# Kernel tuning notes

Measured on AMD Instinct MI355X. Metric: run time of the kernel, lower is better.

The kernel has to match this reference:

```python
import jax, jax.numpy as jnp
import numpy as np

B, N, DIM, CD, K = 8, 4096, 1024, 512, 8192


def setup_inputs() -> dict:
    key = jax.random.key(0)
    k0, k1, k2, k3, k4, k5 = jax.random.split(key, 6)
    s_in = 1.0 / np.sqrt(DIM)
    s_out = 1.0 / np.sqrt(CD)
    return {
        "x": jax.random.normal(k0, (B, N, DIM), dtype=jnp.float32),
        "W_in": jax.random.uniform(k1, (DIM, CD), jnp.float32, -s_in, s_in),
        "b_in": jax.random.uniform(k2, (CD,), jnp.float32, -s_in, s_in),
        "embed": jax.random.normal(k3, (K, CD), dtype=jnp.float32),
        "W_out": jax.random.uniform(k4, (CD, DIM), jnp.float32, -s_out, s_out),
        "b_out": jax.random.uniform(k5, (DIM,), jnp.float32, -s_out, s_out),
    }


def reference(x, W_in, b_in, embed, W_out, b_out):
    # project_in: [B,N,DIM] -> [B,N,CD]
    xp = jnp.einsum('bnd,dc->bnc', x, W_in) + b_in
    flat = xp.reshape(-1, CD)  # [B*N, CD]
    # Euclidean codebook: dist = -||flat - embed||^2 (argmax == nearest code)
    dist = (2.0 * flat @ embed.T
            - jnp.sum(flat * flat, axis=-1, keepdims=True)
            - jnp.sum(embed * embed, axis=-1))  # [B*N, K]
    ind = jnp.argmax(dist, axis=-1)  # [B*N]
    quant = embed[ind].reshape(B, N, CD)
    # commitment loss (training path): mse(quantize.detach(), x_projected)
    commit_loss = jnp.mean(jnp.square(jax.lax.stop_gradient(quant) - xp))
    # straight-through estimator
    quant_st = xp + jax.lax.stop_gradient(quant - xp)
    # project_out: [B,N,CD] -> [B,N,DIM]
    out = jnp.einsum('bnc,cd->bnd', quant_st, W_out) + b_out
    return out, ind.reshape(B, N), commit_loss
```

## Files before the change

### kernel.cpp

```cpp
#include <hip/hip_runtime.h>
#include <hip/hip_bf16.h>
#include <math.h>

#define DIMq 1024
#define CDq  512
#define Kq   8192
#define Mq   32768

#define TAU      1.0e-2f
#define FLAGCAP  4096

typedef __attribute__((ext_vector_type(8))) short bf16x8;
typedef __attribute__((ext_vector_type(4))) float f32x4;
typedef __attribute__((ext_vector_type(4))) unsigned short u16x4;

__device__ __forceinline__ ushort bf16rne(float v) {
  unsigned u = __float_as_uint(v);
  return (ushort)((u + 0x7FFFu + ((u >> 16) & 1u)) >> 16);
}
__device__ __forceinline__ float bf16tof(ushort h) {
  return __uint_as_float(((unsigned)h) << 16);
}

__global__ __launch_bounds__(256) void embed_conv_kernel(const float* __restrict__ e,
                                                         ushort* __restrict__ eh,
                                                         ushort* __restrict__ el) {
  size_t i = ((size_t)blockIdx.x * 256 + threadIdx.x) * 8;
  float4 v0 = *(const float4*)(e + i);
  float4 v1 = *(const float4*)(e + i + 4);
  float vv[8] = {v0.x, v0.y, v0.z, v0.w, v1.x, v1.y, v1.z, v1.w};
  u16x4 h0, h1, l0, l1;
#pragma unroll
  for (int j = 0; j < 4; ++j) {
    ushort hb = bf16rne(vv[j]);     h0[j] = hb; l0[j] = bf16rne(vv[j] - bf16tof(hb));
    ushort hc = bf16rne(vv[4 + j]); h1[j] = hc; l1[j] = bf16rne(vv[4 + j] - bf16tof(hc));
  }
  *(u16x4*)(eh + i) = h0; *(u16x4*)(eh + i + 4) = h1;
  *(u16x4*)(el + i) = l0; *(u16x4*)(el + i + 4) = l1;
}

__global__ __launch_bounds__(256) void seminorm_kernel(const float* __restrict__ embed,
                                                       float* __restrict__ sem) {
  int wid  = blockIdx.x * 4 + (threadIdx.x >> 6);
  int lane = threadIdx.x & 63;
  const float* e = embed + (size_t)wid * CDq;
  double s = 0.0;
#pragma unroll
  for (int j = 0; j < 2; ++j) {
    float4 v = *(const float4*)(e + j * 256 + lane * 4);
    s += (double)v.x * v.x + (double)v.y * v.y + (double)v.z * v.z + (double)v.w * v.w;
  }
#pragma unroll
  for (int off = 32; off; off >>= 1) s += __shfl_down(s, off, 64);
  if (lane == 0) sem[wid] = (float)(0.5 * s);
}

__global__ __launch_bounds__(256) void proj_in_kernel(
    const float* __restrict__ A, const float* __restrict__ Bw,
    const float* __restrict__ bias, ushort* __restrict__ xph, ushort* __restrict__ xpl) {
  __shared__ float As[16][68];
  __shared__ float Bs[16][132];
  const int t = threadIdx.x, tx = t & 15, ty = t >> 4;
  const int rowBase = blockIdx.y * 64;
  const int colBase = blockIdx.x * 128;
  const int rA = t >> 2, kqA = (t & 3) * 4;
  const int kB = t >> 4, cB = (t & 15) * 8;
  const float* Arow = A + (size_t)(rowBase + rA) * DIMq;
  const float* Bp = Bw + (size_t)kB * CDq + colBase + cB;
  float acc[4][8] = {};
  for (int kt = 0; kt < DIMq; kt += 16) {
    float4 av = *(const float4*)(Arow + kt + kqA);
    float4 b0 = *(const float4*)(Bp + (size_t)kt * CDq);
    float4 b1 = *(const float4*)(Bp + (size_t)kt * CDq + 4);
    __syncthreads();
    As[kqA + 0][rA] = av.x; As[kqA + 1][rA] = av.y;
    As[kqA + 2][rA] = av.z; As[kqA + 3][rA] = av.w;
    *(float4*)&Bs[kB][cB]     = b0;
    *(float4*)&Bs[kB][cB + 4] = b1;
    __syncthreads();
#pragma unroll
    for (int kk = 0; kk < 16; ++kk) {
      float4 a  = *(const float4*)&As[kk][ty * 4];
      float4 p0 = *(const float4*)&Bs[kk][tx * 4];
      float4 p1 = *(const float4*)&Bs[kk][64 + tx * 4];
      float ar[4] = {a.x, a.y, a.z, a.w};
      float br[8] = {p0.x, p0.y, p0.z, p0.w, p1.x, p1.y, p1.z, p1.w};
#pragma unroll
      for (int i = 0; i < 4; ++i)
#pragma unroll
        for (int j = 0; j < 8; ++j) acc[i][j] = fmaf(ar[i], br[j], acc[i][j]);
    }
  }
  float4 bi0 = *(const float4*)(bias + colBase + tx * 4);
  float4 bi1 = *(const float4*)(bias + colBase + 64 + tx * 4);
  float bb[8] = {bi0.x, bi0.y, bi0.z, bi0.w, bi1.x, bi1.y, bi1.z, bi1.w};
#pragma unroll
  for (int i = 0; i < 4; ++i) {
    size_t row = rowBase + ty * 4 + i;
    u16x4 h0, h1, l0, l1;
#pragma unroll
    for (int j = 0; j < 4; ++j) {
      float v0 = acc[i][j] + bb[j];
      float v1 = acc[i][4 + j] + bb[4 + j];
      ushort hb = bf16rne(v0); h0[j] = hb; l0[j] = bf16rne(v0 - bf16tof(hb));
      ushort hc = bf16rne(v1); h1[j] = hc; l1[j] = bf16rne(v1 - bf16tof(hc));
    }
    size_t o0 = row * CDq + colBase + tx * 4;
    *(u16x4*)(xph + o0) = h0; *(u16x4*)(xph + o0 + 64) = h1;
    *(u16x4*)(xpl + o0) = l0; *(u16x4*)(xpl + o0 + 64) = l1;
  }
}

__global__ __launch_bounds__(256) void proj_out_kernel(
    const float* __restrict__ A, const float* __restrict__ Bw,
    const float* __restrict__ bias, float* __restrict__ C,
    const int* __restrict__ gidx) {
  __shared__ float As[16][68];
  __shared__ float Bs[16][132];
  const int t = threadIdx.x, tx = t & 15, ty = t >> 4;
  const int rowBase = blockIdx.y * 64;
  const int colBase = blockIdx.x * 128;
  const int rA = t >> 2, kqA = (t & 3) * 4;
  const int kB = t >> 4, cB = (t & 15) * 8;
  const float* Arow = A + (size_t)gidx[rowBase + rA] * CDq;
  const float* Bp = Bw + (size_t)kB * DIMq + colBase + cB;
  float acc[4][8] = {};
  for (int kt = 0; kt < CDq; kt += 16) {
    float4 av = *(const float4*)(Arow + kt + kqA);
    float4 b0 = *(const float4*)(Bp + (size_t)kt * DIMq);
    float4 b1 = *(const float4*)(Bp + (size_t)kt * DIMq + 4);
    __syncthreads();
    As[kqA + 0][rA] = av.x; As[kqA + 1][rA] = av.y;
    As[kqA + 2][rA] = av.z; As[kqA + 3][rA] = av.w;
    *(float4*)&Bs[kB][cB]     = b0;
    *(float4*)&Bs[kB][cB + 4] = b1;
    __syncthreads();
#pragma unroll
    for (int kk = 0; kk < 16; ++kk) {
      float4 a  = *(const float4*)&As[kk][ty * 4];
      float4 p0 = *(const float4*)&Bs[kk][tx * 4];
      float4 p1 = *(const float4*)&Bs[kk][64 + tx * 4];
      float ar[4] = {a.x, a.y, a.z, a.w};
      float br[8] = {p0.x, p0.y, p0.z, p0.w, p1.x, p1.y, p1.z, p1.w};
#pragma unroll
      for (int i = 0; i < 4; ++i)
#pragma unroll
        for (int j = 0; j < 8; ++j) acc[i][j] = fmaf(ar[i], br[j], acc[i][j]);
    }
  }
  float4 bi0 = *(const float4*)(bias + colBase + tx * 4);
  float4 bi1 = *(const float4*)(bias + colBase + 64 + tx * 4);
#pragma unroll
  for (int i = 0; i < 4; ++i) {
    int row = rowBase + ty * 4 + i;
    float4 o0 = {acc[i][0] + bi0.x, acc[i][1] + bi0.y, acc[i][2] + bi0.z, acc[i][3] + bi0.w};
    float4 o1 = {acc[i][4] + bi1.x, acc[i][5] + bi1.y, acc[i][6] + bi1.z, acc[i][7] + bi1.w};
    *(float4*)(C + (size_t)row * DIMq + colBase + tx * 4)      = o0;
    *(float4*)(C + (size_t)row * DIMq + colBase + 64 + tx * 4) = o1;
  }
}

__global__ __launch_bounds__(256) void dist_mfma_kernel(
    const ushort* __restrict__ xph, const ushort* __restrict__ xpl,
    const ushort* __restrict__ eh,  const ushort* __restrict__ el,
    const float* __restrict__ sem,
    float* __restrict__ pb1, float* __restrict__ pb2, int* __restrict__ pidx) {
  __shared__ __align__(16) char smem[65536];
  const int t = threadIdx.x;
  const int wave = t >> 6, lane = t & 63;
  const int wm = wave >> 1, wn = wave & 1;
  const int lx = lane & 15, lg = lane >> 4;
  const int rb = (int)blockIdx.x >> 1, hpart = (int)blockIdx.x & 1;
  const size_t arow0 = (size_t)rb * 128;
  const int code0 = hpart * 4096;

  size_t aoff[2], boff[2];
#pragma unroll
  for (int s = 0; s < 2; ++s) {
    int p = t + s * 256;
    int r = p >> 2;
    int c = (p & 3) ^ ((r >> 1) & 3);
    aoff[s] = (arow0 + r) * CDq + c * 8;
    boff[s] = ((size_t)code0 + r) * CDq + c * 8;
  }
  int offm[4], offn[4];
#pragma unroll
  for (int f = 0; f < 4; ++f) {
    int rm = wm * 64 + f * 16 + lx;
    offm[f] = rm * 64 + ((lg ^ ((rm >> 1) & 3)) * 16);
    int rn = wn * 64 + f * 16 + lx;
    offn[f] = rn * 64 + ((lg ^ ((rn >> 1) & 3)) * 16);
  }

  float b1[16], b2[16]; int ic[16];
#pragma unroll
  for (int s = 0; s < 16; ++s) { b1[s] = -INFINITY; b2[s] = -INFINITY; ic[s] = 0; }

#define STAGE(BUFB, TL, K0)                                                              \
  {                                                                                      \
    char* _bs = smem + (BUFB);                                                           \
    size_t _tb = (size_t)(TL) * 65536 + (K0);                                            \
    _Pragma("unroll")                                                                    \
    for (int s = 0; s < 2; ++s) {                                                        \
      int _p16 = (t + s * 256) * 16;                                                     \
      __builtin_amdgcn_global_load_lds(                                                  \
        (const __attribute__((address_space(1))) unsigned int*)(xph + aoff[s] + (K0)),   \
        (__attribute__((address_space(3))) unsigned int*)(_bs + _p16), 16, 0, 0);        \
      __builtin_amdgcn_global_load_lds(                                                  \
        (const __attribute__((address_space(1))) unsigned int*)(xpl + aoff[s] + (K0)),   \
        (__attribute__((address_space(3))) unsigned int*)(_bs + 8192 + _p16), 16, 0, 0); \
      __builtin_amdgcn_global_load_lds(                                                  \
        (const __attribute__((address_space(1))) unsigned int*)(eh + boff[s] + _tb),     \
        (__attribute__((address_space(3))) unsigned int*)(_bs + 16384 + _p16), 16, 0, 0);\
      __builtin_amdgcn_global_load_lds(                                                  \
        (const __attribute__((address_space(1))) unsigned int*)(el + boff[s] + _tb),     \
        (__attribute__((address_space(3))) unsigned int*)(_bs + 24576 + _p16), 16, 0, 0);\
    }                                                                                    \
  }

  int buf = 0;
  STAGE(0, 0, 0)
#pragma unroll 1
  for (int tile = 0; tile < 32; ++tile) {
    f32x4 acc[4][4];
#pragma unroll
    for (int i = 0; i < 4; ++i)
#pragma unroll
      for (int j = 0; j < 4; ++j) acc[i][j] = (f32x4){0.f, 0.f, 0.f, 0.f};
#pragma unroll 1
    for (int kt = 0; kt < 16; ++kt) {
      __syncthreads();
      int nt = tile, nk = kt + 1;
      if (nk == 16) { nt = tile + 1; nk = 0; }
      if (nt < 32) STAGE((buf ^ 1) * 32768, nt, nk * 32)
      const char* bs = smem + buf * 32768;
      bf16x8 ah[4], al_[4], bh[4], bl_[4];
#pragma unroll
      for (int f = 0; f < 4; ++f) {
        ah[f]  = *(const bf16x8*)(bs + offm[f]);
        al_[f] = *(const bf16x8*)(bs + 8192 + offm[f]);
        bh[f]  = *(const bf16x8*)(bs + 16384 + offn[f]);
        bl_[f] = *(const bf16x8*)(bs + 24576 + offn[f]);
      }
#pragma unroll
      for (int i = 0; i < 4; ++i)
#pragma unroll
        for (int j = 0; j < 4; ++j) {
          acc[i][j] = __builtin_amdgcn_mfma_f32_16x16x32_bf16(ah[i],  bh[j],  acc[i][j], 0, 0, 0);
          acc[i][j] = __builtin_amdgcn_mfma_f32_16x16x32_bf16(ah[i],  bl_[j], acc[i][j], 0, 0, 0);
          acc[i][j] = __builtin_amdgcn_mfma_f32_16x16x32_bf16(al_[i], bh[j],  acc[i][j], 0, 0, 0);
        }
      buf ^= 1;
    }
#pragma unroll
    for (int nf = 0; nf < 4; ++nf) {
      int code = code0 + tile * 128 + wn * 64 + nf * 16 + lx;
      float sv = sem[code];
#pragma unroll
      for (int mf = 0; mf < 4; ++mf)
#pragma unroll
        for (int q = 0; q < 4; ++q) {
          float s = acc[mf][nf][q] - sv;
          int sl = mf * 4 + q;
          if (s > b1[sl]) { b2[sl] = b1[sl]; b1[sl] = s; ic[sl] = code; }
          else if (s > b2[sl]) b2[sl] = s;
        }
    }
  }
#undef STAGE

#pragma unroll
  for (int s = 0; s < 16; ++s) {
#pragma unroll
    for (int m = 1; m < 16; m <<= 1) {
      float o1 = __shfl_xor(b1[s], m, 16);
      float o2 = __shfl_xor(b2[s], m, 16);
      int   oi = __shfl_xor(ic[s], m, 16);
      bool ow = (o1 > b1[s]) || (o1 == b1[s] && oi < ic[s]);
      float l1 = ow ? b1[s] : o1;
      float w2 = ow ? o2 : b2[s];
      if (ow) { b1[s] = o1; ic[s] = oi; }
      b2[s] = fmaxf(w2, l1);
    }
  }
  __syncthreads();
  float* rb1 = (float*)smem;
  float* rb2 = (float*)(smem + 1024);
  int*   ric = (int*)(smem + 2048);
  if (lx == 0) {
#pragma unroll
    for (int mf = 0; mf < 4; ++mf)
#pragma unroll
      for (int q = 0; q < 4; ++q) {
        int r64 = mf * 16 + lg * 4 + q;
        int o = wm * 128 + r64 * 2 + wn;
        int sl = mf * 4 + q;
        rb1[o] = b1[sl]; rb2[o] = b2[sl]; ric[o] = ic[sl];
      }
  }
  __syncthreads();
  if (t < 128) {
    int o0 = t * 2;
    float a1 = rb1[o0], a2 = rb2[o0]; int ai = ric[o0];
    float c1 = rb1[o0 + 1], c2 = rb2[o0 + 1]; int ci = ric[o0 + 1];
    float g1, g2; int gi;
    if (c1 > a1 || (c1 == a1 && ci < ai)) { g1 = c1; gi = ci; g2 = fmaxf(c2, a1); }
    else                                   { g1 = a1; gi = ai; g2 = fmaxf(a2, c1); }
    size_t o = (size_t)hpart * Mq + rb * 128 + t;
    pb1[o] = g1; pb2[o] = g2; pidx[o] = gi;
  }
}

__global__ __launch_bounds__(256) void merge_final_kernel(
    const float* __restrict__ pb1, const float* __restrict__ pb2, const int* __restrict__ pidx,
    int* __restrict__ ind, float* __restrict__ ind_f,
    int* __restrict__ flag_list, int* __restrict__ flag_cnt) {
  int row = blockIdx.x * 256 + threadIdx.x;
  if (row >= Mq) return;
  float a1 = pb1[row], a2 = pb2[row]; int ai = pidx[row];
  float c1 = pb1[Mq + row], c2 = pb2[Mq + row]; int ci = pidx[Mq + row];
  float g1, g2; int gi;
  if (c1 > a1 || (c1 == a1 && ci < ai)) { g1 = c1; gi = ci; g2 = fmaxf(c2, a1); }
  else                                   { g1 = a1; gi = ai; g2 = fmaxf(a2, c1); }
  ind[row] = gi;
  ind_f[row] = (float)gi;
  if (g1 - g2 < TAU) {
    int pos = atomicAdd(flag_cnt, 1);
    if (pos < FLAGCAP) flag_list[pos] = row;
  }
}

__global__ __launch_bounds__(256) void rescue_kernel(
    const float* __restrict__ x, const float* __restrict__ W_in,
    const float* __restrict__ b_in, const float* __restrict__ embed,
    int* __restrict__ ind, float* __restrict__ ind_f,
    const int* __restrict__ flag_list, const int* __restrict__ flag_cnt) {
  __shared__ double xps[CDq];
  __shared__ double rb[256];
  __shared__ int ri[256];
  int cnt = *flag_cnt; if (cnt > FLAGCAP) cnt = FLAGCAP;
  for (int f = blockIdx.x; f < cnt; f += gridDim.x) {
    int row = flag_list[f];
    const float* xr = x + (size_t)row * DIMq;
    for (int c = threadIdx.x; c < CDq; c += 256) {
      double s0 = 0, s1 = 0;
      const float* wc = W_in + c;
      for (int d = 0; d < DIMq; d += 2) {
        s0 += (double)xr[d]     * (double)wc[(size_t)d * CDq];
        s1 += (double)xr[d + 1] * (double)wc[(size_t)(d + 1) * CDq];
      }
      xps[c] = s0 + s1 + (double)b_in[c];
    }
    __syncthreads();
    double best = -1e300; int bi = 0;
    for (int c0 = threadIdx.x; c0 < Kq; c0 += 256) {
      const float* e = embed + (size_t)c0 * CDq;
      double s0 = 0, s1 = 0, s2 = 0, s3 = 0;
      for (int d = 0; d < CDq; d += 4) {
        double e0 = e[d], e1 = e[d + 1], e2 = e[d + 2], e3 = e[d + 3];
        s0 += e0 * (xps[d]     - 0.5 * e0);
        s1 += e1 * (xps[d + 1] - 0.5 * e1);
        s2 += e2 * (xps[d + 2] - 0.5 * e2);
        s3 += e3 * (xps[d + 3] - 0.5 * e3);
      }
      double s = (s0 + s1) + (s2 + s3);
      if (s > best) { best = s; bi = c0; }
    }
    rb[threadIdx.x] = best; ri[threadIdx.x] = bi;
    __syncthreads();
    if (threadIdx.x == 0) {
      double g = -1e300; int gi = 0;
      for (int q = 0; q < 256; ++q)
        if (rb[q] > g || (rb[q] == g && ri[q] < gi)) { g = rb[q]; gi = ri[q]; }
      ind[row] = gi;
      ind_f[row] = (float)gi;
    }
    __syncthreads();
  }
}

__global__ __launch_bounds__(256) void loss_kernel(const ushort* __restrict__ xph,
                                                   const ushort* __restrict__ xpl,
                                                   const float* __restrict__ embed,
                                                   const int* __restrict__ ind,
                                                   float* __restrict__ partials) {
  int b = blockIdx.x;
  float s = 0.f;
  for (int r0 = 0; r0 < 32; ++r0) {
    int row = b * 32 + r0;
    const ushort* xh = xph + (size_t)row * CDq;
    const ushort* xl = xpl + (size_t)row * CDq;
    const float* er = embed + (size_t)ind[row] * CDq;
    for (int c = threadIdx.x; c < CDq; c += 256) {
      float d = er[c] - (bf16tof(xh[c]) + bf16tof(xl[c]));
      s = fmaf(d, d, s);
    }
  }
  __shared__ float red[256];
  red[threadIdx.x] = s; __syncthreads();
  for (int off = 128; off; off >>= 1) {
    if (threadIdx.x < off) red[threadIdx.x] += red[threadIdx.x + off];
    __syncthreads();
  }
  if (threadIdx.x == 0) partials[b] = red[0];
}

__global__ __launch_bounds__(256) void loss_final_kernel(const float* __restrict__ partials,
                                                         float* __restrict__ out_loss) {
  __shared__ double red[256];
  double s = 0;
  for (int i = threadIdx.x; i < 1024; i += 256) s += (double)partials[i];
  red[threadIdx.x] = s; __syncthreads();
  for (int off = 128; off; off >>= 1) {
    if (threadIdx.x < off) red[threadIdx.x] += red[threadIdx.x + off];
    __syncthreads();
  }
  if (threadIdx.x == 0) *out_loss = (float)(red[0] / 16777216.0);
}

extern "C" void kernel_launch(void* const* d_in, const int* in_sizes, int n_in,
                              void* d_out, int out_size, void* d_ws, size_t ws_size,
                              hipStream_t stream) {
  const float* x     = (const float*)d_in[0];
  const float* W_in  = (const float*)d_in[1];
  const float* b_in  = (const float*)d_in[2];
  const float* embed = (const float*)d_in[3];
  const float* W_out = (const float*)d_in[4];
  const float* b_out = (const float*)d_in[5];

  char* ob = (char*)d_out;
  float*  out      = (float*)d_out;
  ushort* xph      = (ushort*)ob;
  ushort* xpl      = (ushort*)(ob + (size_t)(32u << 20));
  ushort* eh       = (ushort*)(ob + (size_t)(64u << 20));
  ushort* el       = (ushort*)(ob + (size_t)(72u << 20));
  float*  pb1      = (float*)(ob + (size_t)(80u << 20));
  float*  pb2      = (float*)(ob + (size_t)(81u << 20));
  int*    pidx     = (int*)  (ob + (size_t)(82u << 20));
  float*  ind_f    = out + (size_t)Mq * DIMq;
  float*  loss_out = ind_f + Mq;

  char* ws = (char*)d_ws;
  int*   flag_cnt  = (int*)ws;
  int*   ind       = (int*)(ws + 64);
  int*   flag_list = (int*)(ws + 64 + (size_t)Mq * 4);
  float* sem       = (float*)(ws + 64 + (size_t)Mq * 4 + FLAGCAP * 4);
  float* partials  = sem + Kq;

  (void)hipMemsetAsync(flag_cnt, 0, 4, stream);
  embed_conv_kernel<<<(Kq * CDq) / (256 * 8), 256, 0, stream>>>(embed, eh, el);
  seminorm_kernel<<<Kq / 4, 256, 0, stream>>>(embed, sem);
  proj_in_kernel<<<dim3(CDq / 128, Mq / 64), 256, 0, stream>>>(x, W_in, b_in, xph, xpl);
  dist_mfma_kernel<<<512, 256, 0, stream>>>(xph, xpl, eh, el, sem, pb1, pb2, pidx);
  merge_final_kernel<<<Mq / 256, 256, 0, stream>>>(pb1, pb2, pidx, ind, ind_f, flag_list, flag_cnt);
  rescue_kernel<<<256, 256, 0, stream>>>(x, W_in, b_in, embed, ind, ind_f, flag_list, flag_cnt);
  loss_kernel<<<1024, 256, 0, stream>>>(xph, xpl, embed, ind, partials);
  loss_final_kernel<<<1, 256, 0, stream>>>(partials, loss_out);
  proj_out_kernel<<<dim3(DIMq / 128, Mq / 64), 256, 0, stream>>>(embed, W_out, b_out, out, ind);
}
```

Before: 2.952 ms.

## Move projections to split-bf16 MFMA, precompute codebook projection, and rework dist tiling

proj_in moves from an fp32 FMA GEMM to a 3-term split-bf16 MFMA GEMM that reads pre-transposed weights. Since the output rows are codebook rows, it precomputes embed@W_out+b_out once per code and gathers rows by index instead of running an M×CD×DIM GEMM. It also splits the dist kernel into four code partitions without double buffering, merges four partials, and vectorizes the loss kernel. The trade-offs are bf16x3 precision in place of fp32, extra transpose kernels, and a dependence on workspace size for the EW buffer.

Result: faster. 2.713 ms (-8.1%).

```diff
diff --git a/kernel.cpp b/kernel.cpp
--- a/kernel.cpp
+++ b/kernel.cpp
@@ -9,6 +9,7 @@
 
 #define TAU      1.0e-2f
 #define FLAGCAP  4096
+#define MiB      (1u << 20)
 
 typedef __attribute__((ext_vector_type(8))) short bf16x8;
 typedef __attribute__((ext_vector_type(4))) float f32x4;
@@ -21,6 +22,11 @@
 __device__ __forceinline__ float bf16tof(ushort h) {
   return __uint_as_float(((unsigned)h) << 16);
 }
+
+#define GL16(gp, lp)                                                       \
+  __builtin_amdgcn_global_load_lds(                                        \
+      (const __attribute__((address_space(1))) unsigned int*)(gp),         \
+      (__attribute__((address_space(3))) unsigned int*)(lp), 16, 0, 0)
 
 __global__ __launch_bounds__(256) void embed_conv_kernel(const float* __restrict__ e,
                                                          ushort* __restrict__ eh,
@@ -55,109 +61,207 @@
   if (lane == 0) sem[wid] = (float)(0.5 * s);
 }
 
-__global__ __launch_bounds__(256) void proj_in_kernel(
-    const float* __restrict__ A, const float* __restrict__ Bw,
-    const float* __restrict__ bias, ushort* __restrict__ xph, ushort* __restrict__ xpl) {
-  __shared__ float As[16][68];
-  __shared__ float Bs[16][132];
-  const int t = threadIdx.x, tx = t & 15, ty = t >> 4;
-  const int rowBase = blockIdx.y * 64;
-  const int colBase = blockIdx.x * 128;
-  const int rA = t >> 2, kqA = (t & 3) * 4;
-  const int kB = t >> 4, cB = (t & 15) * 8;
-  const float* Arow = A + (size_t)(rowBase + rA) * DIMq;
-  const float* Bp = Bw + (size_t)kB * CDq + colBase + cB;
-  float acc[4][8] = {};
-  for (int kt = 0; kt < DIMq; kt += 16) {
-    float4 av = *(const float4*)(Arow + kt + kqA);
-    float4 b0 = *(const float4*)(Bp + (size_t)kt * CDq);
-    float4 b1 = *(const float4*)(Bp + (size_t)kt * CDq + 4);
-    __syncthreads();
-    As[kqA + 0][rA] = av.x; As[kqA + 1][rA] = av.y;
-    As[kqA + 2][rA] = av.z; As[kqA + 3][rA] = av.w;
-    *(float4*)&Bs[kB][cB]     = b0;
-    *(float4*)&Bs[kB][cB + 4] = b1;
-    __syncthreads();
-#pragma unroll
-    for (int kk = 0; kk < 16; ++kk) {
-      float4 a  = *(const float4*)&As[kk][ty * 4];
-      float4 p0 = *(const float4*)&Bs[kk][tx * 4];
-      float4 p1 = *(const float4*)&Bs[kk][64 + tx * 4];
-      float ar[4] = {a.x, a.y, a.z, a.w};
-      float br[8] = {p0.x, p0.y, p0.z, p0.w, p1.x, p1.y, p1.z, p1.w};
-#pragma unroll
-      for (int i = 0; i < 4; ++i)
-#pragma unroll
-        for (int j = 0; j < 8; ++j) acc[i][j] = fmaf(ar[i], br[j], acc[i][j]);
-    }
-  }
-  float4 bi0 = *(const float4*)(bias + colBase + tx * 4);
-  float4 bi1 = *(const float4*)(bias + colBase + 64 + tx * 4);
-  float bb[8] = {bi0.x, bi0.y, bi0.z, bi0.w, bi1.x, bi1.y, bi1.z, bi1.w};
-#pragma unroll
-  for (int i = 0; i < 4; ++i) {
-    size_t row = rowBase + ty * 4 + i;
-    u16x4 h0, h1, l0, l1;
-#pragma unroll
-    for (int j = 0; j < 4; ++j) {
-      float v0 = acc[i][j] + bb[j];
-      float v1 = acc[i][4 + j] + bb[4 + j];
-      ushort hb = bf16rne(v0); h0[j] = hb; l0[j] = bf16rne(v0 - bf16tof(hb));
-      ushort hc = bf16rne(v1); h1[j] = hc; l1[j] = bf16rne(v1 - bf16tof(hc));
-    }
-    size_t o0 = row * CDq + colBase + tx * 4;
-    *(u16x4*)(xph + o0) = h0; *(u16x4*)(xph + o0 + 64) = h1;
-    *(u16x4*)(xpl + o0) = l0; *(u16x4*)(xpl + o0 + 64) = l1;
-  }
-}
-
-__global__ __launch_bounds__(256) void proj_out_kernel(
-    const float* __restrict__ A, const float* __restrict__ Bw,
-    const float* __restrict__ bias, float* __restrict__ C,
-    const int* __restrict__ gidx) {
-  __shared__ float As[16][68];
-  __shared__ float Bs[16][132];
-  const int t = threadIdx.x, tx = t & 15, ty = t >> 4;
-  const int rowBase = blockIdx.y * 64;
-  const int colBase = blockIdx.x * 128;
-  const int rA = t >> 2, kqA = (t & 3) * 4;
-  const int kB = t >> 4, cB = (t & 15) * 8;
-  const float* Arow = A + (size_t)gidx[rowBase + rA] * CDq;
-  const float* Bp = Bw + (size_t)kB * DIMq + colBase + cB;
-  float acc[4][8] = {};
-  for (int kt = 0; kt < CDq; kt += 16) {
-    float4 av = *(const float4*)(Arow + kt + kqA);
-    float4 b0 = *(const float4*)(Bp + (size_t)kt * DIMq);
-    float4 b1 = *(const float4*)(Bp + (size_t)kt * DIMq + 4);
-    __syncthreads();
-    As[kqA + 0][rA] = av.x; As[kqA + 1][rA] = av.y;
-    As[kqA + 2][rA] = av.z; As[kqA + 3][rA] = av.w;
-    *(float4*)&Bs[kB][cB]     = b0;
-    *(float4*)&Bs[kB][cB + 4] = b1;
-    __syncthreads();
-#pragma unroll
-    for (int kk = 0; kk < 16; ++kk) {
-      float4 a  = *(const float4*)&As[kk][ty * 4];
-      float4 p0 = *(const float4*)&Bs[kk][tx * 4];
-      float4 p1 = *(const float4*)&Bs[kk][64 + tx * 4];
-      float ar[4] = {a.x, a.y, a.z, a.w};
-      float br[8] = {p0.x, p0.y, p0.z, p0.w, p1.x, p1.y, p1.z, p1.w};
-#pragma unroll
-      for (int i = 0; i < 4; ++i)
-#pragma unroll
-        for (int j = 0; j < 8; ++j) acc[i][j] = fmaf(ar[i], br[j], acc[i][j]);
-    }
-  }
-  float4 bi0 = *(const float4*)(bias + colBase + tx * 4);
-  float4 bi1 = *(const float4*)(bias + colBase + 64 + tx * 4);
-#pragma unroll
-  for (int i = 0; i < 4; ++i) {
-    int row = rowBase + ty * 4 + i;
-    float4 o0 = {acc[i][0] + bi0.x, acc[i][1] + bi0.y, acc[i][2] + bi0.z, acc[i][3] + bi0.w};
-    float4 o1 = {acc[i][4] + bi1.x, acc[i][5] + bi1.y, acc[i][6] + bi1.z, acc[i][7] + bi1.w};
-    *(float4*)(C + (size_t)row * DIMq + colBase + tx * 4)      = o0;
-    *(float4*)(C + (size_t)row * DIMq + colBase + 64 + tx * 4) = o1;
-  }
+__global__ __launch_bounds__(256) void transpose_split_kernel(
+    const float* __restrict__ src, ushort* __restrict__ dh, ushort* __restrict__ dl,
+    int R, int C) {
+  __shared__ float ts[64][65];
+  int c0 = blockIdx.x * 64, r0 = blockIdx.y * 64;
+#pragma unroll
+  for (int i = 0; i < 16; ++i) {
+    int idx = threadIdx.x + i * 256; int r = idx >> 6, c = idx & 63;
+    ts[r][c] = src[(size_t)(r0 + r) * C + c0 + c];
+  }
+  __syncthreads();
+#pragma unroll
+  for (int i = 0; i < 16; ++i) {
+    int idx = threadIdx.x + i * 256; int a = idx >> 6, b = idx & 63;
+    float v = ts[b][a];
+    ushort h = bf16rne(v);
+    size_t o = (size_t)(c0 + a) * R + r0 + b;
+    dh[o] = h; dl[o] = bf16rne(v - bf16tof(h));
+  }
+}
+
+
+__global__ __launch_bounds__(256) void proj_in_mfma_kernel(
+    const float* __restrict__ x, const ushort* __restrict__ Wth,
+    const ushort* __restrict__ Wtl, const float* __restrict__ bias,
+    ushort* __restrict__ xph, ushort* __restrict__ xpl) {
+  __shared__ __align__(16) char smem[32768];
+  const int t = threadIdx.x;
+  const int wave = t >> 6, lane = t & 63;
+  const int wm = wave >> 1, wn = wave & 1;
+  const int lx = lane & 15, lg = lane >> 4;
+  const int colBase = (int)blockIdx.x * 128;
+  const size_t row0 = (size_t)blockIdx.y * 128;
+
+  int rS[2], cS[2];
+#pragma unroll
+  for (int s = 0; s < 2; ++s) {
+    int p = t + s * 256; rS[s] = p >> 2; cS[s] = (p & 3) ^ ((rS[s] >> 1) & 3);
+  }
+  size_t bbase[2];
+#pragma unroll
+  for (int s = 0; s < 2; ++s) bbase[s] = (size_t)(colBase + rS[s]) * DIMq + cS[s] * 8;
+
+  int offm[4], offn[4];
+#pragma unroll
+  for (int f = 0; f < 4; ++f) {
+    int sw = (lg ^ ((lx >> 1) & 3)) * 16;
+    offm[f] = (wm * 64 + f * 16 + lx) * 64 + sw;
+    offn[f] = (wn * 64 + f * 16 + lx) * 64 + sw;
+  }
+
+  f32x4 acc[4][4];
+#pragma unroll
+  for (int i = 0; i < 4; ++i)
+#pragma unroll
+    for (int j = 0; j < 4; ++j) acc[i][j] = (f32x4){0.f, 0.f, 0.f, 0.f};
+
+#pragma unroll 1
+  for (int kt = 0; kt < DIMq / 32; ++kt) {
+    float4 f0[2], f1[2];
+#pragma unroll
+    for (int s = 0; s < 2; ++s) {
+      const float* src = x + (row0 + rS[s]) * DIMq + kt * 32 + cS[s] * 8;
+      f0[s] = *(const float4*)src; f1[s] = *(const float4*)(src + 4);
+    }
+    __syncthreads();
+#pragma unroll
+    for (int s = 0; s < 2; ++s) {
+      int p16 = (t + s * 256) * 16;
+      GL16(Wth + bbase[s] + kt * 32, smem + 16384 + p16);
+      GL16(Wtl + bbase[s] + kt * 32, smem + 24576 + p16);
+      float ff[8] = {f0[s].x, f0[s].y, f0[s].z, f0[s].w, f1[s].x, f1[s].y, f1[s].z, f1[s].w};
+      union { bf16x8 v; ushort u[8]; } H, L;
+#pragma unroll
+      for (int j = 0; j < 8; ++j) {
+        ushort h = bf16rne(ff[j]); H.u[j] = h; L.u[j] = bf16rne(ff[j] - bf16tof(h));
+      }
+      *(bf16x8*)(smem + p16) = H.v;
+      *(bf16x8*)(smem + 8192 + p16) = L.v;
+    }
+    __syncthreads();
+    bf16x8 ah[4], al_[4], bh[4], bl_[4];
+#pragma unroll
+    for (int f = 0; f < 4; ++f) {
+      ah[f]  = *(const bf16x8*)(smem + offm[f]);
+      al_[f] = *(const bf16x8*)(smem + 8192 + offm[f]);
+      bh[f]  = *(const bf16x8*)(smem + 16384 + offn[f]);
+      bl_[f] = *(const bf16x8*)(smem + 24576 + offn[f]);
+    }
+#pragma unroll
+    for (int i = 0; i < 4; ++i)
+#pragma unroll
+      for (int j = 0; j < 4; ++j) {
+        acc[i][j] = __builtin_amdgcn_mfma_f32_16x16x32_bf16(ah[i],  bh[j],  acc[i][j], 0, 0, 0);
+        acc[i][j] = __builtin_amdgcn_mfma_f32_16x16x32_bf16(ah[i],  bl_[j], acc[i][j], 0, 0, 0);
+        acc[i][j] = __builtin_amdgcn_mfma_f32_16x16x32_bf16(al_[i], bh[j],  acc[i][j], 0, 0, 0);
+      }
+  }
+#pragma unroll
+  for (int nf = 0; nf < 4; ++nf) {
+    int col = colBase + wn * 64 + nf * 16 + lx;
+    float bv = bias[col];
+#pragma unroll
+    for (int mf = 0; mf < 4; ++mf)
+#pragma unroll
+      for (int q = 0; q < 4; ++q) {
+        size_t row = row0 + wm * 64 + mf * 16 + lg * 4 + q;
+        float v = acc[mf][nf][q] + bv;
+        ushort h = bf16rne(v);
+        xph[row * CDq + col] = h;
+        xpl[row * CDq + col] = bf16rne(v - bf16tof(h));
+      }
+  }
+}
+
+__global__ __launch_bounds__(256) void ew_mfma_kernel(
+    const ushort* __restrict__ eh, const ushort* __restrict__ el,
+    const ushort* __restrict__ Woth, const ushort* __restrict__ Wotl,
+    const float* __restrict__ bias, float* __restrict__ EW) {
+  __shared__ __align__(16) char smem[32768];
+  const int t = threadIdx.x;
+  const int wave = t >> 6, lane = t & 63;
+  const int wm = wave >> 1, wn = wave & 1;
+  const int lx = lane & 15, lg = lane >> 4;
+  const int colBase = (int)blockIdx.x * 128;
+  const size_t row0 = (size_t)blockIdx.y * 128;
+
+  int rS[2], cS[2];
+#pragma unroll
+  for (int s = 0; s < 2; ++s) {
+    int p = t + s * 256; rS[s] = p >> 2; cS[s] = (p & 3) ^ ((rS[s] >> 1) & 3);
+  }
+  size_t abase[2], bbase[2];
+#pragma unroll
+  for (int s = 0; s < 2; ++s) {
+    abase[s] = (row0 + rS[s]) * CDq + cS[s] * 8;
+    bbase[s] = (size_t)(colBase + rS[s]) * CDq + cS[s] * 8;
+  }
+  int offm[4], offn[4];
+#pragma unroll
+  for (int f = 0; f < 4; ++f) {
+    int sw = (lg ^ ((lx >> 1) & 3)) * 16;
+    offm[f] = (wm * 64 + f * 16 + lx) * 64 + sw;
+    offn[f] = (wn * 64 + f * 16 + lx) * 64 + sw;
+  }
+  f32x4 acc[4][4];
+#pragma unroll
+  for (int i = 0; i < 4; ++i)
+#pragma unroll
+    for (int j = 0; j < 4; ++j) acc[i][j] = (f32x4){0.f, 0.f, 0.f, 0.f};
+
+#pragma unroll 1
+  for (int kt = 0; kt < CDq / 32; ++kt) {
+    __syncthreads();
+#pragma unroll
+    for (int s = 0; s < 2; ++s) {
+      int p16 = (t + s * 256) * 16;
+      GL16(eh   + abase[s] + kt * 32, smem + p16);
+      GL16(el   + abase[s] + kt * 32, smem + 8192 + p16);
+      GL16(Woth + bbase[s] + kt * 32, smem + 16384 + p16);
+      GL16(Wotl + bbase[s] + kt * 32, smem + 24576 + p16);
+    }
+    __syncthreads();
+    bf16x8 ah[4], al_[4], bh[4], bl_[4];
+#pragma unroll
+    for (int f = 0; f < 4; ++f) {
+      ah[f]  = *(const bf16x8*)(smem + offm[f]);
+      al_[f] = *(const bf16x8*)(smem + 8192 + offm[f]);
+      bh[f]  = *(const bf16x8*)(smem + 16384 + offn[f]);
+      bl_[f] = *(const bf16x8*)(smem + 24576 + offn[f]);
+    }
+#pragma unroll
+    for (int i = 0; i < 4; ++i)
+#pragma unroll
+      for (int j = 0; j < 4; ++j) {
+        acc[i][j] = __builtin_amdgcn_mfma_f32_16x16x32_bf16(ah[i],  bh[j],  acc[i][j], 0, 0, 0);
+        acc[i][j] = __builtin_amdgcn_mfma_f32_16x16x32_bf16(ah[i],  bl_[j], acc[i][j], 0, 0, 0);
+        acc[i][j] = __builtin_amdgcn_mfma_f32_16x16x32_bf16(al_[i], bh[j],  acc[i][j], 0, 0, 0);
+      }
+  }
+#pragma unroll
+  for (int nf = 0; nf < 4; ++nf) {
+    int col = colBase + wn * 64 + nf * 16 + lx;
+    float bv = bias[col];
+#pragma unroll
+    for (int mf = 0; mf < 4; ++mf)
+#pragma unroll
+      for (int q = 0; q < 4; ++q) {
+        size_t row = row0 + wm * 64 + mf * 16 + lg * 4 + q;
+        EW[row * DIMq + col] = acc[mf][nf][q] + bv;
+      }
+  }
+}
+
+__global__ __launch_bounds__(256) void gather_out_kernel(const float* __restrict__ EW,
+                                                         const int* __restrict__ ind,
+                                                         float* __restrict__ out) {
+  int row = blockIdx.x;
+  const float4* src = (const float4*)(EW + (size_t)ind[row] * DIMq);
+  float4* dst = (float4*)(out + (size_t)row * DIMq);
+  dst[threadIdx.x] = src[threadIdx.x];
 }
 
 __global__ __launch_bounds__(256) void dist_mfma_kernel(
@@ -165,82 +269,65 @@
     const ushort* __restrict__ eh,  const ushort* __restrict__ el,
     const float* __restrict__ sem,
     float* __restrict__ pb1, float* __restrict__ pb2, int* __restrict__ pidx) {
-  __shared__ __align__(16) char smem[65536];
+  __shared__ __align__(16) char smem[32768];
   const int t = threadIdx.x;
   const int wave = t >> 6, lane = t & 63;
   const int wm = wave >> 1, wn = wave & 1;
   const int lx = lane & 15, lg = lane >> 4;
-  const int rb = (int)blockIdx.x >> 1, hpart = (int)blockIdx.x & 1;
+  const int rb = (int)blockIdx.x >> 2, part = (int)blockIdx.x & 3;
   const size_t arow0 = (size_t)rb * 128;
-  const int code0 = hpart * 4096;
-
-  size_t aoff[2], boff[2];
+  const int code0 = part * 2048;
+
+  int rS[2], cS[2];
 #pragma unroll
   for (int s = 0; s < 2; ++s) {
-    int p = t + s * 256;
-    int r = p >> 2;
-    int c = (p & 3) ^ ((r >> 1) & 3);
-    aoff[s] = (arow0 + r) * CDq + c * 8;
-    boff[s] = ((size_t)code0 + r) * CDq + c * 8;
+    int p = t + s * 256; rS[s] = p >> 2; cS[s] = (p & 3) ^ ((rS[s] >> 1) & 3);
+  }
+  size_t abase[2], bbase[2];
+#pragma unroll
+  for (int s = 0; s < 2; ++s) {
+    abase[s] = (arow0 + rS[s]) * CDq + cS[s] * 8;
+    bbase[s] = ((size_t)code0 + rS[s]) * CDq + cS[s] * 8;
   }
   int offm[4], offn[4];
 #pragma unroll
   for (int f = 0; f < 4; ++f) {
-    int rm = wm * 64 + f * 16 + lx;
-    offm[f] = rm * 64 + ((lg ^ ((rm >> 1) & 3)) * 16);
-    int rn = wn * 64 + f * 16 + lx;
-    offn[f] = rn * 64 + ((lg ^ ((rn >> 1) & 3)) * 16);
+    int sw = (lg ^ ((lx >> 1) & 3)) * 16;
+    offm[f] = (wm * 64 + f * 16 + lx) * 64 + sw;
+    offn[f] = (wn * 64 + f * 16 + lx) * 64 + sw;
   }
 
   float b1[16], b2[16]; int ic[16];
 #pragma unroll
   for (int s = 0; s < 16; ++s) { b1[s] = -INFINITY; b2[s] = -INFINITY; ic[s] = 0; }
 
-#define STAGE(BUFB, TL, K0)                                                              \
-  {                                                                                      \
-    char* _bs = smem + (BUFB);                                                           \
-    size_t _tb = (size_t)(TL) * 65536 + (K0);                                            \
-    _Pragma("unroll")                                                                    \
-    for (int s = 0; s < 2; ++s) {                                                        \
-      int _p16 = (t + s * 256) * 16;                                                     \
-      __builtin_amdgcn_global_load_lds(                                                  \
-        (const __attribute__((address_space(1))) unsigned int*)(xph + aoff[s] + (K0)),   \
-        (__attribute__((address_space(3))) unsigned int*)(_bs + _p16), 16, 0, 0);        \
-      __builtin_amdgcn_global_load_lds(                                                  \
-        (const __attribute__((address_space(1))) unsigned int*)(xpl + aoff[s] + (K0)),   \
-        (__attribute__((address_space(3))) unsigned int*)(_bs + 8192 + _p16), 16, 0, 0); \
-      __builtin_amdgcn_global_load_lds(                                                  \
-        (const __attribute__((address_space(1))) unsigned int*)(eh + boff[s] + _tb),     \
-        (__attribute__((address_space(3))) unsigned int*)(_bs + 16384 + _p16), 16, 0, 0);\
-      __builtin_amdgcn_global_load_lds(                                                  \
-        (const __attribute__((address_space(1))) unsigned int*)(el + boff[s] + _tb),     \
-        (__attribute__((address_space(3))) unsigned int*)(_bs + 24576 + _p16), 16, 0, 0);\
-    }                                                                                    \
-  }
-
-  int buf = 0;
-  STAGE(0, 0, 0)
 #pragma unroll 1
-  for (int tile = 0; tile < 32; ++tile) {
+  for (int tile = 0; tile < 16; ++tile) {
     f32x4 acc[4][4];
 #pragma unroll
     for (int i = 0; i < 4; ++i)
 #pragma unroll
       for (int j = 0; j < 4; ++j) acc[i][j] = (f32x4){0.f, 0.f, 0.f, 0.f};
+    const size_t tb = (size_t)tile * (128 * CDq);
 #pragma unroll 1
     for (int kt = 0; kt < 16; ++kt) {
       __syncthreads();
-      int nt = tile, nk = kt + 1;
-      if (nk == 16) { nt = tile + 1; nk = 0; }
-      if (nt < 32) STAGE((buf ^ 1) * 32768, nt, nk * 32)
-      const char* bs = smem + buf * 32768;
+#pragma unroll
+      for (int s = 0; s < 2; ++s) {
+        int p16 = (t + s * 256) * 16;
+        GL16(xph + abase[s] + kt * 32,      smem + p16);
+        GL16(xpl + abase[s] + kt * 32,      smem + 8192 + p16);
+        GL16(eh  + bbase[s] + tb + kt * 32, smem + 16384 + p16);
+        GL16(el  + bbase[s] + tb + kt * 32, smem + 24576 + p16);
+      }
+      __syncthreads();
       bf16x8 ah[4], al_[4], bh[4], bl_[4];
 #pragma unroll
       for (int f = 0; f < 4; ++f) {
-        ah[f]  = *(const bf16x8*)(bs + offm[f]);
-        al_[f] = *(const bf16x8*)(bs + 8192 + offm[f]);
-        bh[f]  = *(const bf16x8*)(bs + 16384 + offn[f]);
-        bl_[f] = *(const bf16x8*)(bs + 24576 + offn[f]);
+        ah[f]  = *(const bf16x8*)(smem + offm[f]);
+        al_[f] = *(const bf16x8*)(smem + 8192 + offm[f]);
+        bh[f]  = *(const bf16x8*)(smem + 16384 + offn[f]);
+        bl_[f] = *(const bf16x8*)(smem + 24576 + offn[f]);
       }
 #pragma unroll
       for (int i = 0; i < 4; ++i)
@@ -250,7 +337,6 @@
           acc[i][j] = __builtin_amdgcn_mfma_f32_16x16x32_bf16(ah[i],  bl_[j], acc[i][j], 0, 0, 0);
           acc[i][j] = __builtin_amdgcn_mfma_f32_16x16x32_bf16(al_[i], bh[j],  acc[i][j], 0, 0, 0);
         }
-      buf ^= 1;
     }
 #pragma unroll
     for (int nf = 0; nf < 4; ++nf) {
@@ -267,7 +353,6 @@
         }
     }
   }
-#undef STAGE
 
 #pragma unroll
   for (int s = 0; s < 16; ++s) {
@@ -306,7 +391,7 @@
     float g1, g2; int gi;
     if (c1 > a1 || (c1 == a1 && ci < ai)) { g1 = c1; gi = ci; g2 = fmaxf(c2, a1); }
     else                                   { g1 = a1; gi = ai; g2 = fmaxf(a2, c1); }
-    size_t o = (size_t)hpart * Mq + rb * 128 + t;
+    size_t o = (size_t)part * Mq + arow0 + t;
     pb1[o] = g1; pb2[o] = g2; pidx[o] = gi;
   }
 }
@@ -317,11 +402,14 @@
     int* __restrict__ flag_list, int* __restrict__ flag_cnt) {
   int row = blockIdx.x * 256 + threadIdx.x;
   if (row >= Mq) return;
-  float a1 = pb1[row], a2 = pb2[row]; int ai = pidx[row];
-  float c1 = pb1[Mq + row], c2 = pb2[Mq + row]; int ci = pidx[Mq + row];
-  float g1, g2; int gi;
-  if (c1 > a1 || (c1 == a1 && ci < ai)) { g1 = c1; gi = ci; g2 = fmaxf(c2, a1); }
-  else                                   { g1 = a1; gi = ai; g2 = fmaxf(a2, c1); }
+  float g1 = pb1[row], g2 = pb2[row]; int gi = pidx[row];
+#pragma unroll
+  for (int part = 1; part < 4; ++part) {
+    float c1 = pb1[(size_t)part * Mq + row], c2 = pb2[(size_t)part * Mq + row];
+    int ci = pidx[(size_t)part * Mq + row];
+    if (c1 > g1) { float og1 = g1; g1 = c1; gi = ci; g2 = fmaxf(og1, c2); }
+    else         { g2 = fmaxf(g2, c1); }
+  }
   ind[row] = gi;
   ind_f[row] = (float)gi;
   if (g1 - g2 < TAU) {
@@ -384,25 +472,30 @@
                                                    const float* __restrict__ embed,
                                                    const int* __restrict__ ind,
                                                    float* __restrict__ partials) {
-  int b = blockIdx.x;
+  int wave = threadIdx.x >> 6, lane = threadIdx.x & 63;
   float s = 0.f;
-  for (int r0 = 0; r0 < 32; ++r0) {
-    int row = b * 32 + r0;
-    const ushort* xh = xph + (size_t)row * CDq;
-    const ushort* xl = xpl + (size_t)row * CDq;
-    const float* er = embed + (size_t)ind[row] * CDq;
-    for (int c = threadIdx.x; c < CDq; c += 256) {
-      float d = er[c] - (bf16tof(xh[c]) + bf16tof(xl[c]));
-      s = fmaf(d, d, s);
-    }
-  }
-  __shared__ float red[256];
-  red[threadIdx.x] = s; __syncthreads();
-  for (int off = 128; off; off >>= 1) {
-    if (threadIdx.x < off) red[threadIdx.x] += red[threadIdx.x + off];
-    __syncthreads();
-  }
-  if (threadIdx.x == 0) partials[b] = red[0];
+#pragma unroll 1
+  for (int i = 0; i < 8; ++i) {
+    int row = blockIdx.x * 32 + wave * 8 + i;
+    size_t o = (size_t)row * CDq + lane * 8;
+    u16x4 h0 = *(const u16x4*)(xph + o), h1 = *(const u16x4*)(xph + o + 4);
+    u16x4 l0 = *(const u16x4*)(xpl + o), l1 = *(const u16x4*)(xpl + o + 4);
+    const float* er = embed + (size_t)ind[row] * CDq + lane * 8;
+    float4 e0 = *(const float4*)er, e1 = *(const float4*)(er + 4);
+    float ee[8] = {e0.x, e0.y, e0.z, e0.w, e1.x, e1.y, e1.z, e1.w};
+#pragma unroll
+    for (int j = 0; j < 4; ++j) {
+      float d0 = ee[j]     - (bf16tof(h0[j]) + bf16tof(l0[j]));
+      float d1 = ee[4 + j] - (bf16tof(h1[j]) + bf16tof(l1[j]));
+      s = fmaf(d0, d0, s); s = fmaf(d1, d1, s);
+    }
+  }
+#pragma unroll
+  for (int off = 32; off; off >>= 1) s += __shfl_down(s, off, 64);
+  __shared__ float red[4];
+  if (lane == 0) red[wave] = s;
+  __syncthreads();
+  if (threadIdx.x == 0) partials[blockIdx.x] = red[0] + red[1] + red[2] + red[3];
 }
 
 __global__ __launch_bounds__(256) void loss_final_kernel(const float* __restrict__ partials,
@@ -416,6 +509,55 @@
     __syncthreads();
   }
   if (threadIdx.x == 0) *out_loss = (float)(red[0] / 16777216.0);
+}
+
+__global__ __launch_bounds__(256) void proj_out_f32_kernel(
+    const float* __restrict__ A, const float* __restrict__ Bw,
+    const float* __restrict__ bias, float* __restrict__ C,
+    const int* __restrict__ gidx) {
+  __shared__ float As[16][68];
+  __shared__ float Bs[16][132];
+  const int t = threadIdx.x, tx = t & 15, ty = t >> 4;
+  const int rowBase = blockIdx.y * 64;
+  const int colBase = blockIdx.x * 128;
+  const int rA = t >> 2, kqA = (t & 3) * 4;
+  const int kB = t >> 4, cB = (t & 15) * 8;
+  const float* Arow = A + (size_t)gidx[rowBase + rA] * CDq;
+  const float* Bp = Bw + (size_t)kB * DIMq + colBase + cB;
+  float acc[4][8] = {};
+  for (int kt = 0; kt < CDq; kt += 16) {
+    float4 av = *(const float4*)(Arow + kt + kqA);
+    float4 b0 = *(const float4*)(Bp + (size_t)kt * DIMq);
+    float4 b1 = *(const float4*)(Bp + (size_t)kt * DIMq + 4);
+    __syncthreads();
+    As[kqA + 0][rA] = av.x; As[kqA + 1][rA] = av.y;
+    As[kqA + 2][rA] = av.z; As[kqA + 3][rA] = av.w;
+    *(float4*)&Bs[kB][cB]     = b0;
+    *(float4*)&Bs[kB][cB + 4] = b1;
+    __syncthreads();
+#pragma unroll
+    for (int kk = 0; kk < 16; ++kk) {
+      float4 a  = *(const float4*)&As[kk][ty * 4];
+      float4 p0 = *(const float4*)&Bs[kk][tx * 4];
+      float4 p1 = *(const float4*)&Bs[kk][64 + tx * 4];
+      float ar[4] = {a.x, a.y, a.z, a.w};
+      float br[8] = {p0.x, p0.y, p0.z, p0.w, p1.x, p1.y, p1.z, p1.w};
+#pragma unroll
+      for (int i = 0; i < 4; ++i)
+#pragma unroll
+        for (int j = 0; j < 8; ++j) acc[i][j] = fmaf(ar[i], br[j], acc[i][j]);
+    }
+  }
+  float4 bi0 = *(const float4*)(bias + colBase + tx * 4);
+  float4 bi1 = *(const float4*)(bias + colBase + 64 + tx * 4);
+#pragma unroll
+  for (int i = 0; i < 4; ++i) {
+    int row = rowBase + ty * 4 + i;
+    float4 o0 = {acc[i][0] + bi0.x, acc[i][1] + bi0.y, acc[i][2] + bi0.z, acc[i][3] + bi0.w};
+    float4 o1 = {acc[i][4] + bi1.x, acc[i][5] + bi1.y, acc[i][6] + bi1.z, acc[i][7] + bi1.w};
+    *(float4*)(C + (size_t)row * DIMq + colBase + tx * 4)      = o0;
+    *(float4*)(C + (size_t)row * DIMq + colBase + 64 + tx * 4) = o1;
+  }
 }
 
 extern "C" void kernel_launch(void* const* d_in, const int* in_sizes, int n_in,
@@ -429,15 +571,19 @@
   const float* b_out = (const float*)d_in[5];
 
   char* ob = (char*)d_out;
-  float*  out      = (float*)d_out;
-  ushort* xph      = (ushort*)ob;
-  ushort* xpl      = (ushort*)(ob + (size_t)(32u << 20));
-  ushort* eh       = (ushort*)(ob + (size_t)(64u << 20));
-  ushort* el       = (ushort*)(ob + (size_t)(72u << 20));
-  float*  pb1      = (float*)(ob + (size_t)(80u << 20));
-  float*  pb2      = (float*)(ob + (size_t)(81u << 20));
-  int*    pidx     = (int*)  (ob + (size_t)(82u << 20));
-  float*  ind_f    = out + (size_t)Mq * DIMq;
+  float*  out   = (float*)d_out;
+  ushort* xph   = (ushort*)ob;
+  ushort* xpl   = (ushort*)(ob + (size_t)32 * MiB);
+  ushort* eh    = (ushort*)(ob + (size_t)64 * MiB);
+  ushort* el    = (ushort*)(ob + (size_t)72 * MiB);
+  ushort* Wth   = (ushort*)(ob + (size_t)80 * MiB);
+  ushort* Wtl   = (ushort*)(ob + (size_t)81 * MiB);
+  ushort* Woth  = (ushort*)(ob + (size_t)82 * MiB);
+  ushort* Wotl  = (ushort*)(ob + (size_t)83 * MiB);
+  float*  pb1   = (float*)(ob + (size_t)84 * MiB);
+  float*  pb2   = pb1 + 4 * (size_t)Mq;
+  int*    pidx  = (int*)(pb2 + 4 * (size_t)Mq);
+  float*  ind_f = out + (size_t)Mq * DIMq;
   float*  loss_out = ind_f + Mq;
 
   char* ws = (char*)d_ws;
@@ -446,15 +592,24 @@
   int*   flag_list = (int*)(ws + 64 + (size_t)Mq * 4);
   float* sem       = (float*)(ws + 64 + (size_t)Mq * 4 + FLAGCAP * 4);
   float* partials  = sem + Kq;
+  float* EW        = (float*)(ws + (size_t)1 * MiB);
+  const bool big_ws = ws_size >= (size_t)36 * MiB;
 
   (void)hipMemsetAsync(flag_cnt, 0, 4, stream);
   embed_conv_kernel<<<(Kq * CDq) / (256 * 8), 256, 0, stream>>>(embed, eh, el);
   seminorm_kernel<<<Kq / 4, 256, 0, stream>>>(embed, sem);
-  proj_in_kernel<<<dim3(CDq / 128, Mq / 64), 256, 0, stream>>>(x, W_in, b_in, xph, xpl);
-  dist_mfma_kernel<<<512, 256, 0, stream>>>(xph, xpl, eh, el, sem, pb1, pb2, pidx);
+  transpose_split_kernel<<<dim3(CDq / 64, DIMq / 64), 256, 0, stream>>>(W_in, Wth, Wtl, DIMq, CDq);
+  transpose_split_kernel<<<dim3(DIMq / 64, CDq / 64), 256, 0, stream>>>(W_out, Woth, Wotl, CDq, DIMq);
+  if (big_ws)
+    ew_mfma_kernel<<<dim3(DIMq / 128, Kq / 128), 256, 0, stream>>>(eh, el, Woth, Wotl, b_out, EW);
+  proj_in_mfma_kernel<<<dim3(CDq / 128, Mq / 128), 256, 0, stream>>>(x, Wth, Wtl, b_in, xph, xpl);
+  dist_mfma_kernel<<<Mq / 128 * 4, 256, 0, stream>>>(xph, xpl, eh, el, sem, pb1, pb2, pidx);
   merge_final_kernel<<<Mq / 256, 256, 0, stream>>>(pb1, pb2, pidx, ind, ind_f, flag_list, flag_cnt);
   rescue_kernel<<<256, 256, 0, stream>>>(x, W_in, b_in, embed, ind, ind_f, flag_list, flag_cnt);
-  loss_kernel<<<1024, 256, 0, stream>>>(xph, xpl, embed, ind, partials);
+  loss_kernel<<<Mq / 32, 256, 0, stream>>>(xph, xpl, embed, ind, partials);
   loss_final_kernel<<<1, 256, 0, stream>>>(partials, loss_out);
-  proj_out_kernel<<<dim3(DIMq / 128, Mq / 64), 256, 0, stream>>>(embed, W_out, b_out, out, ind);
-}
+  if (big_ws)
+    gather_out_kernel<<<Mq, 256, 0, stream>>>(EW, ind, out);
+  else
+    proj_out_f32_kernel<<<dim3(DIMq / 128, Mq / 64), 256, 0, stream>>>(embed, W_out, b_out, out, ind);
+}
```
